# Kernel optimization log

Measured on AMD Instinct MI355X. Metric: run time of the kernel, lower is better.

Reference implementation:

```python
import jax, jax.numpy as jnp
import numpy as np

D_MODEL = 1024
N_HEADS = 16
D_K = D_MODEL // N_HEADS
BATCH = 2
SEQ = 2048


def setup_inputs() -> dict:
    key = jax.random.key(0)
    ks = jax.random.split(key, 9)
    s = 1.0 / np.sqrt(D_MODEL)
    x = jax.random.normal(ks[0], (BATCH, SEQ, D_MODEL), dtype=jnp.float32)
    # nn.Linear params: weight [out, in], bias [out]
    w_q = jax.random.uniform(ks[1], (D_MODEL, D_MODEL), jnp.float32, -s, s)
    b_q = jax.random.uniform(ks[2], (D_MODEL,), jnp.float32, -s, s)
    w_k = jax.random.uniform(ks[3], (D_MODEL, D_MODEL), jnp.float32, -s, s)
    b_k = jax.random.uniform(ks[4], (D_MODEL,), jnp.float32, -s, s)
    w_v = jax.random.uniform(ks[5], (D_MODEL, D_MODEL), jnp.float32, -s, s)
    b_v = jax.random.uniform(ks[6], (D_MODEL,), jnp.float32, -s, s)
    w_o = jax.random.uniform(ks[7], (D_MODEL, D_MODEL), jnp.float32, -s, s)
    b_o = jax.random.uniform(ks[8], (D_MODEL,), jnp.float32, -s, s)
    return {"x": x, "w_q": w_q, "b_q": b_q, "w_k": w_k, "b_k": b_k,
            "w_v": w_v, "b_v": b_v, "w_o": w_o, "b_o": b_o}


def reference(x, w_q, b_q, w_k, b_k, w_v, b_v, w_o, b_o):
    B, S, _ = x.shape
    # Linear projections, then split heads: [B, H, S, d_k]
    def proj(w, b):
        y = jnp.einsum('bsd,ed->bse', x, w) + b
        return y.reshape(B, S, N_HEADS, D_K).transpose(0, 2, 1, 3)
    q = proj(w_q, b_q)
    k = proj(w_k, b_k)
    v = proj(w_v, b_v)
    scores = jnp.einsum('bhqd,bhkd->bhqk', q, k) / jnp.sqrt(jnp.float32(D_K))
    attn = jax.nn.softmax(scores, axis=-1)  # dropout is identity in eval mode
    out = jnp.einsum('bhqk,bhkd->bhqd', attn, v)
    out = out.transpose(0, 2, 1, 3).reshape(B, S, D_MODEL)
    out = jnp.einsum('bsd,ed->bse', out, w_o) + b_o
    return out, attn
```

## Files before the change

### kernel.cpp

```cpp
#include <hip/hip_runtime.h>
#include <hip/hip_bf16.h>
#include <stdint.h>


typedef __attribute__((ext_vector_type(4))) float f32x4;
typedef __attribute__((ext_vector_type(8))) short s16x8;
typedef __attribute__((ext_vector_type(4))) unsigned int u32x4;
typedef __attribute__((ext_vector_type(4))) unsigned short u16x4;

#define MFMA(a, b, c) __builtin_amdgcn_mfma_f32_16x16x32_bf16((a), (b), (c), 0, 0, 0)

#if __has_builtin(__builtin_amdgcn_exp2f)
#define EXP2(x) __builtin_amdgcn_exp2f(x)
#else
#define EXP2(x) exp2f(x)
#endif

__device__ __forceinline__ unsigned short f2bf(float f) {
    unsigned int u = __float_as_uint(f);
    unsigned int r = (u + 0x7FFFu + ((u >> 16) & 1u)) >> 16;
    return (unsigned short)r;
}
__device__ __forceinline__ unsigned int cvtpk_bf16(float lo, float hi) {
    unsigned int r;
    asm("v_cvt_pk_bf16_f32 %0, %1, %2" : "=v"(r) : "v"(lo), "v"(hi));
    return r;
}

__global__ void convert_kernel(const float* __restrict__ x,
                               const float* __restrict__ wq, const float* __restrict__ wk,
                               const float* __restrict__ wv, const float* __restrict__ wo,
                               unsigned short* __restrict__ xb, unsigned short* __restrict__ wb) {
    size_t g = (size_t)blockIdx.x * blockDim.x + threadIdx.x;
    size_t i4 = g * 4;
    const float* src;
    unsigned short* dst;
    size_t off;
    if (i4 < 4194304) {
        src = x; dst = xb; off = i4;
    } else {
        size_t j = i4 - 4194304;
        int wsel = (int)(j >> 20);
        off = j & 1048575;
        src = (wsel == 0) ? wq : (wsel == 1) ? wk : (wsel == 2) ? wv : wo;
        dst = wb + ((size_t)wsel << 20);
    }
    float4 v = *(const float4*)(src + off);
    u16x4 o;
    o[0] = f2bf(v.x); o[1] = f2bf(v.y); o[2] = f2bf(v.z); o[3] = f2bf(v.w);
    *(u16x4*)(dst + off) = o;
}

__global__ __launch_bounds__(256, 3) void gemm_kernel(
    const unsigned short* __restrict__ A, const unsigned short* __restrict__ B,
    const float* __restrict__ bias_q, const float* __restrict__ bias_k,
    const float* __restrict__ bias_v, int mode,
    unsigned short* __restrict__ Qs, unsigned short* __restrict__ Kb,
    unsigned short* __restrict__ Vt, float* __restrict__ outp) {
    const int t = threadIdx.x;
    const int lane = t & 63;
    const int wv4 = t >> 6;
    const int wr = wv4 >> 1, wc = wv4 & 1;
    const int rowbase = blockIdx.y * 128;
    const int colbase = blockIdx.x * 128;

    __shared__ __align__(16) unsigned short lA[128 * 64];
    __shared__ __align__(16) unsigned short lB[128 * 64];

    const int crow = lane >> 3;
    const int ccol = (lane & 7) * 8;

    f32x4 acc[4][4];
#pragma unroll
    for (int mi = 0; mi < 4; ++mi)
#pragma unroll
        for (int ni = 0; ni < 4; ++ni)
            acc[mi][ni] = (f32x4){0.f, 0.f, 0.f, 0.f};

    const int l15 = lane & 15;
    const int koff = (lane >> 4) * 8;
    const int ar = wr * 64 + l15;
    const int br = wc * 64 + l15;

    for (int kt = 0; kt < 16; ++kt) {
        const int kbase = kt * 64 + ccol;
#pragma unroll
        for (int i = 0; i < 4; ++i) {
            const int c = wv4 * 4 + i;
            const int r = c * 8 + crow;
            __builtin_amdgcn_global_load_lds(
                (const __attribute__((address_space(1))) void*)(A + (size_t)(rowbase + r) * 1024 + kbase),
                (__attribute__((address_space(3))) void*)&lA[c * 512], 16, 0, 0);
            __builtin_amdgcn_global_load_lds(
                (const __attribute__((address_space(1))) void*)(B + (size_t)(colbase + r) * 1024 + kbase),
                (__attribute__((address_space(3))) void*)&lB[c * 512], 16, 0, 0);
        }
        __syncthreads();
#pragma unroll
        for (int kk = 0; kk < 2; ++kk) {
            s16x8 af[4], bf[4];
#pragma unroll
            for (int mi = 0; mi < 4; ++mi)
                af[mi] = *(const s16x8*)&lA[(ar + mi * 16) * 64 + kk * 32 + koff];
#pragma unroll
            for (int ni = 0; ni < 4; ++ni)
                bf[ni] = *(const s16x8*)&lB[(br + ni * 16) * 64 + kk * 32 + koff];
#pragma unroll
            for (int mi = 0; mi < 4; ++mi)
#pragma unroll
                for (int ni = 0; ni < 4; ++ni)
                    acc[mi][ni] = MFMA(af[mi], bf[ni], acc[mi][ni]);
        }
        __syncthreads();
    }

    if (mode == 1) {
#pragma unroll
        for (int ni = 0; ni < 4; ++ni) {
            int n = colbase + wc * 64 + ni * 16 + l15;
            float bv = bias_q[n];
#pragma unroll
            for (int mi = 0; mi < 4; ++mi) {
#pragma unroll
                for (int reg = 0; reg < 4; ++reg) {
                    int m = rowbase + wr * 64 + mi * 16 + (lane >> 4) * 4 + reg;
                    outp[(size_t)m * 1024 + n] = acc[mi][ni][reg] + bv;
                }
            }
        }
    } else {
        const int proj = colbase >> 10;
        const float* bias = (proj == 0) ? bias_q : (proj == 1) ? bias_k : bias_v;
        const float scale = (proj == 0) ? 0.18033688011112042f : 1.0f;
#pragma unroll
        for (int ni = 0; ni < 4; ++ni) {
            int n = colbase + wc * 64 + ni * 16 + l15;
            int nn = n & 1023;
            int h = nn >> 6, d = nn & 63;
            float bv = bias[nn];
#pragma unroll
            for (int mi = 0; mi < 4; ++mi) {
                int m0 = rowbase + wr * 64 + mi * 16 + (lane >> 4) * 4;
                int b = m0 >> 11, s0 = m0 & 2047;
                if (proj == 2) {
                    u16x4 pk;
#pragma unroll
                    for (int reg = 0; reg < 4; ++reg)
                        pk[reg] = f2bf(acc[mi][ni][reg] + bv);
                    int j0 = s0 & 31;
                    int pg = (j0 >> 2) & 3, pn = (j0 >> 4) & 1;
                    int pcol = (s0 & ~31) | (pg << 3) | (pn << 2);
                    *(u16x4*)&Vt[((size_t)(b * 16 + h) * 64 + d) * 2048 + pcol] = pk;
                } else {
                    unsigned short* dstp = (proj == 0) ? Qs : Kb;
#pragma unroll
                    for (int reg = 0; reg < 4; ++reg)
                        dstp[((size_t)(b * 16 + h) * 2048 + (s0 + reg)) * 64 + d] =
                            f2bf((acc[mi][ni][reg] + bv) * scale);
                }
            }
        }
    }
}

__global__ __launch_bounds__(256, 2) void attn_kernel(
    const unsigned short* __restrict__ Qs, const unsigned short* __restrict__ Kb,
    const unsigned short* __restrict__ Vt, float* __restrict__ attn,
    unsigned short* __restrict__ ctx) {
    const int t = threadIdx.x;
    const int lane = t & 63;
    const int l15 = lane & 15;
    const int g = lane >> 4;
    const int g4 = g * 4, g8 = g * 8;
    const int w = t >> 6;
    const int qt = blockIdx.x;
    const int bh = blockIdx.y;
    const int b = bh >> 4, h = bh & 15;

    const unsigned short* Qh = Qs + (size_t)bh * (2048 * 64);
    const unsigned short* Kh = Kb + (size_t)bh * (2048 * 64);
    const unsigned short* Vh = Vt + (size_t)bh * (64 * 2048);
    float* attn_h = attn + (size_t)bh * (2048 * 2048) + (size_t)(qt * 128) * 2048;

    __shared__ float sc[4][32 * 68];

    const int qbase = w * 32;

    s16x8 qf[4];
#pragma unroll
    for (int mi = 0; mi < 2; ++mi)
#pragma unroll
        for (int kk = 0; kk < 2; ++kk)
            qf[mi * 2 + kk] = *(const s16x8*)&Qh[(size_t)(qt * 128 + qbase + mi * 16 + l15) * 64 +
                                                kk * 32 + g8];

    float qsum[2] = {0.f, 0.f};
    for (int kt = 0; kt < 32; ++kt) {
        s16x8 kf[8];
#pragma unroll
        for (int ni = 0; ni < 4; ++ni)
#pragma unroll
            for (int kk = 0; kk < 2; ++kk)
                kf[ni * 2 + kk] =
                    *(const s16x8*)&Kh[(size_t)(kt * 64 + ni * 16 + l15) * 64 + kk * 32 + g8];
        f32x4 sacc[2][4];
#pragma unroll
        for (int mi = 0; mi < 2; ++mi)
#pragma unroll
            for (int ni = 0; ni < 4; ++ni) sacc[mi][ni] = (f32x4){0.f, 0.f, 0.f, 0.f};
#pragma unroll
        for (int kk = 0; kk < 2; ++kk)
#pragma unroll
            for (int mi = 0; mi < 2; ++mi)
#pragma unroll
                for (int ni = 0; ni < 4; ++ni)
                    sacc[mi][ni] = MFMA(kf[ni * 2 + kk], qf[mi * 2 + kk], sacc[mi][ni]);
#pragma unroll
        for (int mi = 0; mi < 2; ++mi) {
            float e = 0.f;
#pragma unroll
            for (int ni = 0; ni < 4; ++ni)
#pragma unroll
                for (int r = 0; r < 4; ++r) e += EXP2(sacc[mi][ni][r]);
            qsum[mi] += e;
        }
    }
    float rl[2];
#pragma unroll
    for (int mi = 0; mi < 2; ++mi) {
        float v = qsum[mi];
        v += __shfl_xor(v, 16);
        v += __shfl_xor(v, 32);
        rl[mi] = 1.0f / v;
    }

    f32x4 oacc[2][4];
#pragma unroll
    for (int mi = 0; mi < 2; ++mi)
#pragma unroll
        for (int db = 0; db < 4; ++db) oacc[mi][db] = (f32x4){0.f, 0.f, 0.f, 0.f};

    for (int kt = 0; kt < 32; ++kt) {
        s16x8 kf[8];
#pragma unroll
        for (int ni = 0; ni < 4; ++ni)
#pragma unroll
            for (int kk = 0; kk < 2; ++kk)
                kf[ni * 2 + kk] =
                    *(const s16x8*)&Kh[(size_t)(kt * 64 + ni * 16 + l15) * 64 + kk * 32 + g8];
        s16x8 vf[8];
#pragma unroll
        for (int db = 0; db < 4; ++db)
#pragma unroll
            for (int ks = 0; ks < 2; ++ks)
                vf[db * 2 + ks] =
                    *(const s16x8*)&Vh[(size_t)(db * 16 + l15) * 2048 + kt * 64 + ks * 32 + g8];
        f32x4 sacc[2][4];
#pragma unroll
        for (int mi = 0; mi < 2; ++mi)
#pragma unroll
            for (int ni = 0; ni < 4; ++ni) sacc[mi][ni] = (f32x4){0.f, 0.f, 0.f, 0.f};
#pragma unroll
        for (int kk = 0; kk < 2; ++kk)
#pragma unroll
            for (int mi = 0; mi < 2; ++mi)
#pragma unroll
                for (int ni = 0; ni < 4; ++ni)
                    sacc[mi][ni] = MFMA(kf[ni * 2 + kk], qf[mi * 2 + kk], sacc[mi][ni]);

        s16x8 pf0, pf1, pf2, pf3;
#pragma unroll
        for (int mi = 0; mi < 2; ++mi) {
            float p[16];
#pragma unroll
            for (int ni = 0; ni < 4; ++ni) {
#pragma unroll
                for (int r = 0; r < 4; ++r) p[ni * 4 + r] = EXP2(sacc[mi][ni][r]) * rl[mi];
                f32x4 pv = {p[ni * 4 + 0], p[ni * 4 + 1], p[ni * 4 + 2], p[ni * 4 + 3]};
                *(f32x4*)&sc[w][(mi * 16 + l15) * 68 + ni * 16 + g4] = pv;
            }
            u32x4 w0, w1;
            w0[0] = cvtpk_bf16(p[0], p[1]);   w0[1] = cvtpk_bf16(p[2], p[3]);
            w0[2] = cvtpk_bf16(p[4], p[5]);   w0[3] = cvtpk_bf16(p[6], p[7]);
            w1[0] = cvtpk_bf16(p[8], p[9]);   w1[1] = cvtpk_bf16(p[10], p[11]);
            w1[2] = cvtpk_bf16(p[12], p[13]); w1[3] = cvtpk_bf16(p[14], p[15]);
            if (mi == 0) { pf0 = *(const s16x8*)&w0; pf1 = *(const s16x8*)&w1; }
            else         { pf2 = *(const s16x8*)&w0; pf3 = *(const s16x8*)&w1; }
        }

#pragma unroll
        for (int i = 0; i < 8; ++i) {
            const int ql = i * 4 + g;
            f32x4 v = *(const f32x4*)&sc[w][ql * 68 + l15 * 4];
            *(f32x4*)&attn_h[(size_t)(qbase + ql) * 2048 + kt * 64 + l15 * 4] = v;
        }

#pragma unroll
        for (int db = 0; db < 4; ++db) {
            oacc[0][db] = MFMA(pf0, vf[db * 2 + 0], oacc[0][db]);
            oacc[0][db] = MFMA(pf1, vf[db * 2 + 1], oacc[0][db]);
            oacc[1][db] = MFMA(pf2, vf[db * 2 + 0], oacc[1][db]);
            oacc[1][db] = MFMA(pf3, vf[db * 2 + 1], oacc[1][db]);
        }
    }

#pragma unroll
    for (int mi = 0; mi < 2; ++mi) {
#pragma unroll
        for (int db = 0; db < 4; ++db) {
#pragma unroll
            for (int r = 0; r < 4; ++r) {
                int q = qt * 128 + qbase + mi * 16 + g4 + r;
                ctx[((size_t)(b * 2048 + q)) * 1024 + h * 64 + db * 16 + l15] =
                    f2bf(oacc[mi][db][r]);
            }
        }
    }
}

extern "C" void kernel_launch(void* const* d_in, const int* in_sizes, int n_in,
                              void* d_out, int out_size, void* d_ws, size_t ws_size,
                              hipStream_t stream) {
    const float* x  = (const float*)d_in[0];
    const float* wq = (const float*)d_in[1];
    const float* bq = (const float*)d_in[2];
    const float* wk = (const float*)d_in[3];
    const float* bk = (const float*)d_in[4];
    const float* wv = (const float*)d_in[5];
    const float* bv = (const float*)d_in[6];
    const float* wo = (const float*)d_in[7];
    const float* bo = (const float*)d_in[8];

    char* ws = (char*)d_ws;
    unsigned short* xb  = (unsigned short*)(ws);
    unsigned short* wb  = (unsigned short*)(ws + 8388608);
    unsigned short* Qsc = (unsigned short*)(ws + 16777216);
    unsigned short* Kb  = (unsigned short*)(ws + 25165824);
    unsigned short* Vt  = (unsigned short*)(ws + 33554432);
    unsigned short* ctx = (unsigned short*)(ws + 41943040);

    float* out  = (float*)d_out;
    float* attn = out + 4194304;

    convert_kernel<<<8192, 256, 0, stream>>>(x, wq, wk, wv, wo, xb, wb);
    gemm_kernel<<<dim3(24, 32), 256, 0, stream>>>(xb, wb, bq, bk, bv, 0,
                                                  Qsc, Kb, Vt, nullptr);
    attn_kernel<<<dim3(16, 32), 256, 0, stream>>>(Qsc, Kb, Vt, attn, ctx);
    gemm_kernel<<<dim3(8, 32), 256, 0, stream>>>(ctx, wb + 3 * 1048576, bo, bo, bo, 1,
                                                 nullptr, nullptr, nullptr, out);
}
```

Measured before the change: 336.4 us.

## Split attention key range across wave pairs with 64-query tiles

Each attention block now covers 64 queries instead of 128. Pairs of waves split each 64-key tile into two 32-key halves, which doubles the grid to 1024 blocks and raises the occupancy target to 4 blocks per CU. Row sums and partial PV outputs are combined through LDS with barriers. The attn probabilities are now stored directly from registers rather than staged through LDS, so the stores are less coalesced (16-byte pieces per lane) in exchange for dropping the LDS round-trip. K and V fragments are also loaded redundantly across more blocks.

```diff
diff --git a/kernel.cpp b/kernel.cpp
--- a/kernel.cpp
+++ b/kernel.cpp
@@ -163,7 +163,7 @@
     }
 }
 
-__global__ __launch_bounds__(256, 2) void attn_kernel(
+__global__ __launch_bounds__(256, 4) void attn_kernel(
     const unsigned short* __restrict__ Qs, const unsigned short* __restrict__ Kb,
     const unsigned short* __restrict__ Vt, float* __restrict__ attn,
     unsigned short* __restrict__ ctx) {
@@ -173,6 +173,7 @@
     const int g = lane >> 4;
     const int g4 = g * 4, g8 = g * 8;
     const int w = t >> 6;
+    const int wc = w & 1, wh = w >> 1;
     const int qt = blockIdx.x;
     const int bh = blockIdx.y;
     const int b = bh >> 4, h = bh & 15;
@@ -180,58 +181,70 @@
     const unsigned short* Qh = Qs + (size_t)bh * (2048 * 64);
     const unsigned short* Kh = Kb + (size_t)bh * (2048 * 64);
     const unsigned short* Vh = Vt + (size_t)bh * (64 * 2048);
-    float* attn_h = attn + (size_t)bh * (2048 * 2048) + (size_t)(qt * 128) * 2048;
-
-    __shared__ float sc[4][32 * 68];
-
-    const int qbase = w * 32;
+    float* attn_h = attn + (size_t)bh * (2048 * 2048) + (size_t)(qt * 64) * 2048;
+
+    __shared__ float lred[2][64];
+    __shared__ float lO[2][32 * 68];
+
+    const int qbase = wh * 32;
 
     s16x8 qf[4];
 #pragma unroll
     for (int mi = 0; mi < 2; ++mi)
 #pragma unroll
         for (int kk = 0; kk < 2; ++kk)
-            qf[mi * 2 + kk] = *(const s16x8*)&Qh[(size_t)(qt * 128 + qbase + mi * 16 + l15) * 64 +
+            qf[mi * 2 + kk] = *(const s16x8*)&Qh[(size_t)(qt * 64 + qbase + mi * 16 + l15) * 64 +
                                                 kk * 32 + g8];
 
     float qsum[2] = {0.f, 0.f};
     for (int kt = 0; kt < 32; ++kt) {
-        s16x8 kf[8];
-#pragma unroll
-        for (int ni = 0; ni < 4; ++ni)
+        s16x8 kf[4];
+#pragma unroll
+        for (int ni = 0; ni < 2; ++ni)
 #pragma unroll
             for (int kk = 0; kk < 2; ++kk)
-                kf[ni * 2 + kk] =
-                    *(const s16x8*)&Kh[(size_t)(kt * 64 + ni * 16 + l15) * 64 + kk * 32 + g8];
-        f32x4 sacc[2][4];
-#pragma unroll
-        for (int mi = 0; mi < 2; ++mi)
-#pragma unroll
-            for (int ni = 0; ni < 4; ++ni) sacc[mi][ni] = (f32x4){0.f, 0.f, 0.f, 0.f};
+                kf[ni * 2 + kk] = *(const s16x8*)&Kh[(size_t)(kt * 64 + wc * 32 + ni * 16 + l15) *
+                                                        64 + kk * 32 + g8];
+        f32x4 sacc[2][2];
+#pragma unroll
+        for (int mi = 0; mi < 2; ++mi)
+#pragma unroll
+            for (int ni = 0; ni < 2; ++ni) sacc[mi][ni] = (f32x4){0.f, 0.f, 0.f, 0.f};
 #pragma unroll
         for (int kk = 0; kk < 2; ++kk)
 #pragma unroll
             for (int mi = 0; mi < 2; ++mi)
 #pragma unroll
-                for (int ni = 0; ni < 4; ++ni)
+                for (int ni = 0; ni < 2; ++ni)
                     sacc[mi][ni] = MFMA(kf[ni * 2 + kk], qf[mi * 2 + kk], sacc[mi][ni]);
 #pragma unroll
         for (int mi = 0; mi < 2; ++mi) {
             float e = 0.f;
 #pragma unroll
-            for (int ni = 0; ni < 4; ++ni)
+            for (int ni = 0; ni < 2; ++ni)
 #pragma unroll
                 for (int r = 0; r < 4; ++r) e += EXP2(sacc[mi][ni][r]);
             qsum[mi] += e;
         }
     }
-    float rl[2];
 #pragma unroll
     for (int mi = 0; mi < 2; ++mi) {
         float v = qsum[mi];
         v += __shfl_xor(v, 16);
         v += __shfl_xor(v, 32);
-        rl[mi] = 1.0f / v;
+        qsum[mi] = v;
+    }
+    if (lane < 16) {
+#pragma unroll
+        for (int mi = 0; mi < 2; ++mi)
+            lred[wc][qbase + mi * 16 + lane] = qsum[mi];
+    }
+    __syncthreads();
+    float rl[2];
+#pragma unroll
+    for (int mi = 0; mi < 2; ++mi) {
+        int q = qbase + mi * 16 + l15;
+        rl[mi] = 1.0f / (lred[0][q] + lred[1][q]);
     }
 
     f32x4 oacc[2][4];
@@ -241,78 +254,79 @@
         for (int db = 0; db < 4; ++db) oacc[mi][db] = (f32x4){0.f, 0.f, 0.f, 0.f};
 
     for (int kt = 0; kt < 32; ++kt) {
-        s16x8 kf[8];
-#pragma unroll
-        for (int ni = 0; ni < 4; ++ni)
+        s16x8 kf[4];
+#pragma unroll
+        for (int ni = 0; ni < 2; ++ni)
 #pragma unroll
             for (int kk = 0; kk < 2; ++kk)
-                kf[ni * 2 + kk] =
-                    *(const s16x8*)&Kh[(size_t)(kt * 64 + ni * 16 + l15) * 64 + kk * 32 + g8];
-        s16x8 vf[8];
+                kf[ni * 2 + kk] = *(const s16x8*)&Kh[(size_t)(kt * 64 + wc * 32 + ni * 16 + l15) *
+                                                        64 + kk * 32 + g8];
+        s16x8 vf[4];
 #pragma unroll
         for (int db = 0; db < 4; ++db)
-#pragma unroll
-            for (int ks = 0; ks < 2; ++ks)
-                vf[db * 2 + ks] =
-                    *(const s16x8*)&Vh[(size_t)(db * 16 + l15) * 2048 + kt * 64 + ks * 32 + g8];
-        f32x4 sacc[2][4];
-#pragma unroll
-        for (int mi = 0; mi < 2; ++mi)
-#pragma unroll
-            for (int ni = 0; ni < 4; ++ni) sacc[mi][ni] = (f32x4){0.f, 0.f, 0.f, 0.f};
+            vf[db] = *(const s16x8*)&Vh[(size_t)(db * 16 + l15) * 2048 + kt * 64 + wc * 32 + g8];
+        f32x4 sacc[2][2];
+#pragma unroll
+        for (int mi = 0; mi < 2; ++mi)
+#pragma unroll
+            for (int ni = 0; ni < 2; ++ni) sacc[mi][ni] = (f32x4){0.f, 0.f, 0.f, 0.f};
 #pragma unroll
         for (int kk = 0; kk < 2; ++kk)
 #pragma unroll
             for (int mi = 0; mi < 2; ++mi)
 #pragma unroll
-                for (int ni = 0; ni < 4; ++ni)
+                for (int ni = 0; ni < 2; ++ni)
                     sacc[mi][ni] = MFMA(kf[ni * 2 + kk], qf[mi * 2 + kk], sacc[mi][ni]);
 
-        s16x8 pf0, pf1, pf2, pf3;
+        s16x8 pf[2];
 #pragma unroll
         for (int mi = 0; mi < 2; ++mi) {
-            float p[16];
-#pragma unroll
-            for (int ni = 0; ni < 4; ++ni) {
-#pragma unroll
-                for (int r = 0; r < 4; ++r) p[ni * 4 + r] = EXP2(sacc[mi][ni][r]) * rl[mi];
+            const int q = qbase + mi * 16 + l15;
+            float p[8];
+#pragma unroll
+            for (int ni = 0; ni < 2; ++ni) {
+                p[ni * 4 + 0] = EXP2(sacc[mi][ni][0]) * rl[mi];
+                p[ni * 4 + 1] = EXP2(sacc[mi][ni][1]) * rl[mi];
+                p[ni * 4 + 2] = EXP2(sacc[mi][ni][2]) * rl[mi];
+                p[ni * 4 + 3] = EXP2(sacc[mi][ni][3]) * rl[mi];
                 f32x4 pv = {p[ni * 4 + 0], p[ni * 4 + 1], p[ni * 4 + 2], p[ni * 4 + 3]};
-                *(f32x4*)&sc[w][(mi * 16 + l15) * 68 + ni * 16 + g4] = pv;
+                *(f32x4*)&attn_h[(size_t)q * 2048 + kt * 64 + wc * 32 + ni * 16 + g4] = pv;
             }
-            u32x4 w0, w1;
-            w0[0] = cvtpk_bf16(p[0], p[1]);   w0[1] = cvtpk_bf16(p[2], p[3]);
-            w0[2] = cvtpk_bf16(p[4], p[5]);   w0[3] = cvtpk_bf16(p[6], p[7]);
-            w1[0] = cvtpk_bf16(p[8], p[9]);   w1[1] = cvtpk_bf16(p[10], p[11]);
-            w1[2] = cvtpk_bf16(p[12], p[13]); w1[3] = cvtpk_bf16(p[14], p[15]);
-            if (mi == 0) { pf0 = *(const s16x8*)&w0; pf1 = *(const s16x8*)&w1; }
-            else         { pf2 = *(const s16x8*)&w0; pf3 = *(const s16x8*)&w1; }
-        }
-
-#pragma unroll
-        for (int i = 0; i < 8; ++i) {
-            const int ql = i * 4 + g;
-            f32x4 v = *(const f32x4*)&sc[w][ql * 68 + l15 * 4];
-            *(f32x4*)&attn_h[(size_t)(qbase + ql) * 2048 + kt * 64 + l15 * 4] = v;
-        }
-
-#pragma unroll
-        for (int db = 0; db < 4; ++db) {
-            oacc[0][db] = MFMA(pf0, vf[db * 2 + 0], oacc[0][db]);
-            oacc[0][db] = MFMA(pf1, vf[db * 2 + 1], oacc[0][db]);
-            oacc[1][db] = MFMA(pf2, vf[db * 2 + 0], oacc[1][db]);
-            oacc[1][db] = MFMA(pf3, vf[db * 2 + 1], oacc[1][db]);
-        }
-    }
-
-#pragma unroll
-    for (int mi = 0; mi < 2; ++mi) {
-#pragma unroll
-        for (int db = 0; db < 4; ++db) {
-#pragma unroll
-            for (int r = 0; r < 4; ++r) {
-                int q = qt * 128 + qbase + mi * 16 + g4 + r;
-                ctx[((size_t)(b * 2048 + q)) * 1024 + h * 64 + db * 16 + l15] =
-                    f2bf(oacc[mi][db][r]);
+            u32x4 pkw;
+            pkw[0] = cvtpk_bf16(p[0], p[1]);
+            pkw[1] = cvtpk_bf16(p[2], p[3]);
+            pkw[2] = cvtpk_bf16(p[4], p[5]);
+            pkw[3] = cvtpk_bf16(p[6], p[7]);
+            pf[mi] = *(const s16x8*)&pkw;
+        }
+#pragma unroll
+        for (int mi = 0; mi < 2; ++mi)
+#pragma unroll
+            for (int db = 0; db < 4; ++db)
+                oacc[mi][db] = MFMA(pf[mi], vf[db], oacc[mi][db]);
+    }
+
+    if (wc == 1) {
+#pragma unroll
+        for (int mi = 0; mi < 2; ++mi)
+#pragma unroll
+            for (int db = 0; db < 4; ++db)
+#pragma unroll
+                for (int r = 0; r < 4; ++r)
+                    lO[wh][(mi * 16 + g4 + r) * 68 + db * 16 + l15] = oacc[mi][db][r];
+    }
+    __syncthreads();
+    if (wc == 0) {
+#pragma unroll
+        for (int mi = 0; mi < 2; ++mi) {
+#pragma unroll
+            for (int db = 0; db < 4; ++db) {
+#pragma unroll
+                for (int r = 0; r < 4; ++r) {
+                    float s = oacc[mi][db][r] + lO[wh][(mi * 16 + g4 + r) * 68 + db * 16 + l15];
+                    int q = qt * 64 + qbase + mi * 16 + g4 + r;
+                    ctx[((size_t)(b * 2048 + q)) * 1024 + h * 64 + db * 16 + l15] = f2bf(s);
+                }
             }
         }
     }
@@ -345,7 +359,7 @@
     convert_kernel<<<8192, 256, 0, stream>>>(x, wq, wk, wv, wo, xb, wb);
     gemm_kernel<<<dim3(24, 32), 256, 0, stream>>>(xb, wb, bq, bk, bv, 0,
                                                   Qsc, Kb, Vt, nullptr);
-    attn_kernel<<<dim3(16, 32), 256, 0, stream>>>(Qsc, Kb, Vt, attn, ctx);
+    attn_kernel<<<dim3(32, 32), 256, 0, stream>>>(Qsc, Kb, Vt, attn, ctx);
     gemm_kernel<<<dim3(8, 32), 256, 0, stream>>>(ctx, wb + 3 * 1048576, bo, bo, bo, 1,
                                                  nullptr, nullptr, nullptr, out);
 }
```

Measured after the change: 332.6 us. About the same (-1.1%).
